# Optimization experiments

Hardware: AMD Instinct MI355X
Metric: run time of the kernel (lower is better)

The kernel has to match this reference:

```python
import jax, jax.numpy as jnp
import numpy as np

B, V, M, C = 1024, 2, 256, 256  # batch, num_vars (must be 2), latent states, categories


def setup_inputs() -> dict:
    key = jax.random.key(0)
    k1, k2, k3 = jax.random.split(key, 3)
    x = jax.random.randint(k1, (B, V), 0, C)
    # input-node tables: per var v, per latent node k, a [M, C] row-normalized table
    W = jax.nn.softmax(jax.random.normal(k2, (V, M, M, C), dtype=jnp.float32), axis=-1)
    # sum-node mixture weights over the M product children
    w_sum = jax.nn.softmax(jax.random.normal(k3, (M,), dtype=jnp.float32))
    return {"x": x, "W": W, "w_sum": w_sum}


def reference(x, W, w_sum):
    # lp[v] has shape [M(k), M(m), B]: log W[v, k, m, x[b, v]]
    # (matches torch: probs[:, x_var].log() per input node, stacked over latent k)
    lp0 = jnp.log(W[0][:, :, x[:, 0]])  # [M, M, B]
    lp1 = jnp.log(W[1][:, :, x[:, 1]])  # [M, M, B]
    prod = lp0 + lp1                    # product nodes, [M(k), M, B]
    # sum node: log( sum_k w_k * exp(prod_k) ) -> [M, B]
    mixed = jnp.log(jnp.einsum('k,kmb->mb', w_sum, jnp.exp(prod)))
    # root: logsumexp over the leading M dim -> [B]
    return jax.nn.logsumexp(mixed, axis=0)
```

## Files before the change

kernel.cpp:

```cpp
#include <hip/hip_runtime.h>
#include <math.h>


#define NBLK    256
#define KCHUNK  256
#define BK      64
#define NITER   (KCHUNK / BK)

typedef float  f32x4  __attribute__((ext_vector_type(4)));
typedef short  bf16x8 __attribute__((ext_vector_type(8)));

static __device__ __forceinline__ short f2bf(float f) {
    unsigned u = __builtin_bit_cast(unsigned, f);
    u += 0x7fffu + ((u >> 16) & 1u);
    return (short)(u >> 16);
}

static __device__ __forceinline__ int swz(int c) {
    return ((c >> 2) & 7) ^ ((c & 1) << 2);
}

__global__ __launch_bounds__(512, 2) void hclt_gemm(
    const int* __restrict__ x, const float* __restrict__ W,
    const float* __restrict__ wsum, float* __restrict__ P)
{
    __shared__ __align__(16) char smem[65536];
    __shared__ int pairs[1024];

    char*  const AsB = smem;
    char*  const BsB = smem + 32768;
    float* const G   = (float*)smem;

    const int  blk   = blockIdx.x;
    const long kbase = (long)blk * KCHUNK;
    const float wk   = wsum[blk];

    const float* __restrict__ Ag = W + kbase * 256;
    const float* __restrict__ Bg = W + 16777216 + kbase * 256;

    const int t    = threadIdx.x;
    const int lane = t & 63;
    const int wv   = t >> 6;

    {
        const int2 p0 = ((const int2*)x)[t];
        const int2 p1 = ((const int2*)x)[t + 512];
        pairs[t]       = (p0.x << 8) | p0.y;
        pairs[t + 512] = (p1.x << 8) | p1.y;
    }

    const int cq = lane * 4;
    const int g0 = wv;

    const int wc0 = (wv & 3) * 64;
    const int wc1 = (wv >> 2) * 128;
    const int ml  = lane & 15;
    const int qd  = lane >> 4;

    f32x4 acc[4][8];
#pragma unroll
    for (int i = 0; i < 4; ++i)
#pragma unroll
        for (int j = 0; j < 8; ++j) acc[i][j] = (f32x4){0.f, 0.f, 0.f, 0.f};

    float4 a4[8], b4[8];

#pragma unroll
    for (int r = 0; r < 8; ++r) {
        a4[r] = *(const float4*)(Ag + (long)(g0 * 8 + r) * 256 + cq);
        b4[r] = *(const float4*)(Bg + (long)(g0 * 8 + r) * 256 + cq);
    }
#pragma unroll
    for (int j = 0; j < 4; ++j) {
        const int c = cq + j;
        bf16x8 av, bv;
#pragma unroll
        for (int r = 0; r < 8; ++r) {
            av[r] = f2bf(((const float*)&a4[r])[j] * wk);
            bv[r] = f2bf(((const float*)&b4[r])[j]);
        }
        const int off = c * 128 + (g0 ^ swz(c)) * 16;
        *(bf16x8*)(AsB + off) = av;
        *(bf16x8*)(BsB + off) = bv;
    }
    __syncthreads();

#pragma unroll
    for (int it = 0; it < NITER; ++it) {
        if (it + 1 < NITER) {
#pragma unroll
            for (int r = 0; r < 8; ++r) {
                a4[r] = *(const float4*)(Ag + (long)((it + 1) * BK + g0 * 8 + r) * 256 + cq);
                b4[r] = *(const float4*)(Bg + (long)((it + 1) * BK + g0 * 8 + r) * 256 + cq);
            }
        }
#pragma unroll
        for (int s = 0; s < 2; ++s) {
            bf16x8 afr[4];
#pragma unroll
            for (int mi = 0; mi < 4; ++mi) {
                const int c = wc0 + mi * 16 + ml;
                afr[mi] = *(const bf16x8*)(AsB + c * 128 + (((s << 2) + qd) ^ swz(c)) * 16);
            }
#pragma unroll
            for (int ni = 0; ni < 8; ++ni) {
                const int c = wc1 + ni * 16 + ml;
                const bf16x8 bfr =
                    *(const bf16x8*)(BsB + c * 128 + (((s << 2) + qd) ^ swz(c)) * 16);
#pragma unroll
                for (int mi = 0; mi < 4; ++mi)
                    acc[mi][ni] = __builtin_amdgcn_mfma_f32_16x16x32_bf16(
                        afr[mi], bfr, acc[mi][ni], 0, 0, 0);
            }
        }
        if (it + 1 < NITER) {
            __syncthreads();
#pragma unroll
            for (int j = 0; j < 4; ++j) {
                const int c = cq + j;
                bf16x8 av, bv;
#pragma unroll
                for (int r = 0; r < 8; ++r) {
                    av[r] = f2bf(((const float*)&a4[r])[j] * wk);
                    bv[r] = f2bf(((const float*)&b4[r])[j]);
                }
                const int off = c * 128 + (g0 ^ swz(c)) * 16;
                *(bf16x8*)(AsB + off) = av;
                *(bf16x8*)(BsB + off) = bv;
            }
            __syncthreads();
        }
    }

    float v0 = 0.f, v1 = 0.f;
#pragma unroll 1
    for (int ph = 0; ph < 8; ++ph) {
        __syncthreads();
        if (wv == ph) {
#pragma unroll
            for (int mi = 0; mi < 4; ++mi)
#pragma unroll
                for (int ni = 0; ni < 8; ++ni)
#pragma unroll
                    for (int r = 0; r < 4; ++r)
                        G[(mi * 16 + qd * 4 + r) * 130 + (ni * 16 + ml)] = acc[mi][ni][r];
        }
        __syncthreads();
        {
            int pr = pairs[t];
            int c0 = pr >> 8, c1 = pr & 255;
            if ((((c0 >> 6) & 3) | ((c1 >> 7) << 2)) == ph)
                v0 = G[(c0 & 63) * 130 + (c1 & 127)];
            pr = pairs[t + 512];
            c0 = pr >> 8; c1 = pr & 255;
            if ((((c0 >> 6) & 3) | ((c1 >> 7) << 2)) == ph)
                v1 = G[(c0 & 63) * 130 + (c1 & 127)];
        }
    }
    P[(size_t)blk * 1024 + t]       = v0;
    P[(size_t)blk * 1024 + 512 + t] = v1;
}

__global__ __launch_bounds__(256) void hclt_finish(
    const float* __restrict__ P, float* __restrict__ out)
{
    const int i = blockIdx.x * 256 + threadIdx.x;
    float s0 = 0.f, s1 = 0.f, s2 = 0.f, s3 = 0.f;
#pragma unroll 8
    for (int s = 0; s < NBLK; s += 4) {
        s0 += P[(size_t)(s + 0) * 1024 + i];
        s1 += P[(size_t)(s + 1) * 1024 + i];
        s2 += P[(size_t)(s + 2) * 1024 + i];
        s3 += P[(size_t)(s + 3) * 1024 + i];
    }
    out[i] = logf((s0 + s1) + (s2 + s3));
}

extern "C" void kernel_launch(void* const* d_in, const int* in_sizes, int n_in,
                              void* d_out, int out_size, void* d_ws, size_t ws_size,
                              hipStream_t stream)
{
    const int*   x    = (const int*)d_in[0];
    const float* W    = (const float*)d_in[1];
    const float* wsum = (const float*)d_in[2];
    float* out = (float*)d_out;

    float* P = (float*)d_ws;

    hclt_gemm<<<dim3(NBLK), 512, 0, stream>>>(x, W, wsum, P);
    hclt_finish<<<dim3(4), 256, 0, stream>>>(P, out);
}
```

Baseline: 220.3 us.

## Split each k-chunk GEMM across two blocks by A-row halves, shrink tiles

Each k-chunk is now handled by two 256-thread blocks, each computing half of the A dimension (128 rows), giving 512 blocks instead of 256. The K tile shrinks to 32 with a new swizzle, and shared memory drops to about 33 KB. The wsum scaling moves from every bf16 conversion to the final gathered values, and the finish kernel is reworked to reduce over 512 partials with a shared-memory reduction across 16 blocks. This aims to raise occupancy and CU coverage on a 256-CU part, at the cost of B-tile loads duplicated across the two blocks of a pair and more synchronisation steps.

Result: slower. 227.5 us (+3.3%).

```diff
diff --git a/kernel.cpp b/kernel.cpp
--- a/kernel.cpp
+++ b/kernel.cpp
@@ -2,9 +2,8 @@
 #include <math.h>
 
 
-#define NBLK    256
 #define KCHUNK  256
-#define BK      64
+#define BK      32
 #define NITER   (KCHUNK / BK)
 
 typedef float  f32x4  __attribute__((ext_vector_type(4)));
@@ -16,44 +15,49 @@
     return (short)(u >> 16);
 }
 
-static __device__ __forceinline__ int swz(int c) {
-    return ((c >> 2) & 7) ^ ((c & 1) << 2);
-}
-
-__global__ __launch_bounds__(512, 2) void hclt_gemm(
+static __device__ __forceinline__ int s2(int c) {
+    return ((c >> 2) ^ ((c & 1) << 1)) & 3;
+}
+
+__global__ __launch_bounds__(256, 2) void hclt_gemm(
     const int* __restrict__ x, const float* __restrict__ W,
     const float* __restrict__ wsum, float* __restrict__ P)
 {
-    __shared__ __align__(16) char smem[65536];
+    __shared__ __align__(16) char smem[33280];
     __shared__ int pairs[1024];
 
-    char*  const AsB = smem;
-    char*  const BsB = smem + 32768;
-    float* const G   = (float*)smem;
-
-    const int  blk   = blockIdx.x;
-    const long kbase = (long)blk * KCHUNK;
-    const float wk   = wsum[blk];
-
-    const float* __restrict__ Ag = W + kbase * 256;
+    char*  const As = smem;
+    char*  const Bs = smem + 8192;
+    float* const G  = (float*)smem;
+
+    const int blk   = blockIdx.x;
+    const int split = ((blk >> 4) << 3) | (blk & 7);
+    const int h     = (blk >> 3) & 1;
+    const long kbase = (long)split * KCHUNK;
+
+    const float* __restrict__ Ag = W + kbase * 256 + h * 128;
     const float* __restrict__ Bg = W + 16777216 + kbase * 256;
 
     const int t    = threadIdx.x;
     const int lane = t & 63;
     const int wv   = t >> 6;
 
-    {
-        const int2 p0 = ((const int2*)x)[t];
-        const int2 p1 = ((const int2*)x)[t + 512];
-        pairs[t]       = (p0.x << 8) | p0.y;
-        pairs[t + 512] = (p1.x << 8) | p1.y;
-    }
-
-    const int cq = lane * 4;
-    const int g0 = wv;
-
-    const int wc0 = (wv & 3) * 64;
-    const int wc1 = (wv >> 2) * 128;
+#pragma unroll
+    for (int jj = 0; jj < 4; ++jj) {
+        const int2 p = ((const int2*)x)[t + 256 * jj];
+        pairs[t + 256 * jj] = (p.x << 8) | p.y;
+    }
+
+    const bool isA = (t < 128);
+    const int  uA  = t;
+    const int  cqA = (uA & 31) * 4;
+    const int  oA  = uA >> 5;
+    const int  vB  = t & 127;
+    const int  cqB = (vB & 63) * 4;
+    const int  oB  = (vB >> 6) * 2;
+
+    const int wc0 = (wv & 1) * 64;
+    const int wc1 = (wv >> 1) * 128;
     const int ml  = lane & 15;
     const int qd  = lane >> 4;
 
@@ -63,78 +67,106 @@
 #pragma unroll
         for (int j = 0; j < 8; ++j) acc[i][j] = (f32x4){0.f, 0.f, 0.f, 0.f};
 
-    float4 a4[8], b4[8];
-
-#pragma unroll
-    for (int r = 0; r < 8; ++r) {
-        a4[r] = *(const float4*)(Ag + (long)(g0 * 8 + r) * 256 + cq);
-        b4[r] = *(const float4*)(Bg + (long)(g0 * 8 + r) * 256 + cq);
-    }
-#pragma unroll
-    for (int j = 0; j < 4; ++j) {
-        const int c = cq + j;
-        bf16x8 av, bv;
-#pragma unroll
-        for (int r = 0; r < 8; ++r) {
-            av[r] = f2bf(((const float*)&a4[r])[j] * wk);
-            bv[r] = f2bf(((const float*)&b4[r])[j]);
-        }
-        const int off = c * 128 + (g0 ^ swz(c)) * 16;
-        *(bf16x8*)(AsB + off) = av;
-        *(bf16x8*)(BsB + off) = bv;
+    float4 pf[16];
+
+    if (isA) {
+#pragma unroll
+        for (int r = 0; r < 8; ++r)
+            pf[r] = *(const float4*)(Ag + (long)(oA * 8 + r) * 256 + cqA);
+    } else {
+#pragma unroll
+        for (int uo = 0; uo < 2; ++uo)
+#pragma unroll
+            for (int r = 0; r < 8; ++r)
+                pf[uo * 8 + r] = *(const float4*)(Bg + (long)((oB + uo) * 8 + r) * 256 + cqB);
+    }
+    if (isA) {
+#pragma unroll
+        for (int j = 0; j < 4; ++j) {
+            const int c = cqA + j;
+            bf16x8 av;
+#pragma unroll
+            for (int r = 0; r < 8; ++r) av[r] = f2bf(((const float*)&pf[r])[j]);
+            *(bf16x8*)(As + c * 64 + ((oA ^ s2(c)) & 3) * 16) = av;
+        }
+    } else {
+#pragma unroll
+        for (int uo = 0; uo < 2; ++uo)
+#pragma unroll
+            for (int j = 0; j < 4; ++j) {
+                const int c = cqB + j;
+                bf16x8 bv;
+#pragma unroll
+                for (int r = 0; r < 8; ++r) bv[r] = f2bf(((const float*)&pf[uo * 8 + r])[j]);
+                *(bf16x8*)(Bs + c * 64 + (((oB + uo) ^ s2(c)) & 3) * 16) = bv;
+            }
     }
     __syncthreads();
 
 #pragma unroll
     for (int it = 0; it < NITER; ++it) {
         if (it + 1 < NITER) {
-#pragma unroll
-            for (int r = 0; r < 8; ++r) {
-                a4[r] = *(const float4*)(Ag + (long)((it + 1) * BK + g0 * 8 + r) * 256 + cq);
-                b4[r] = *(const float4*)(Bg + (long)((it + 1) * BK + g0 * 8 + r) * 256 + cq);
-            }
-        }
-#pragma unroll
-        for (int s = 0; s < 2; ++s) {
-            bf16x8 afr[4];
-#pragma unroll
-            for (int mi = 0; mi < 4; ++mi) {
-                const int c = wc0 + mi * 16 + ml;
-                afr[mi] = *(const bf16x8*)(AsB + c * 128 + (((s << 2) + qd) ^ swz(c)) * 16);
-            }
-#pragma unroll
-            for (int ni = 0; ni < 8; ++ni) {
-                const int c = wc1 + ni * 16 + ml;
-                const bf16x8 bfr =
-                    *(const bf16x8*)(BsB + c * 128 + (((s << 2) + qd) ^ swz(c)) * 16);
-#pragma unroll
-                for (int mi = 0; mi < 4; ++mi)
-                    acc[mi][ni] = __builtin_amdgcn_mfma_f32_16x16x32_bf16(
-                        afr[mi], bfr, acc[mi][ni], 0, 0, 0);
-            }
+            const long k0 = (long)(it + 1) * BK;
+            if (isA) {
+#pragma unroll
+                for (int r = 0; r < 8; ++r)
+                    pf[r] = *(const float4*)(Ag + (k0 + oA * 8 + r) * 256 + cqA);
+            } else {
+#pragma unroll
+                for (int uo = 0; uo < 2; ++uo)
+#pragma unroll
+                    for (int r = 0; r < 8; ++r)
+                        pf[uo * 8 + r] =
+                            *(const float4*)(Bg + (k0 + (oB + uo) * 8 + r) * 256 + cqB);
+            }
+        }
+        bf16x8 afr[4];
+#pragma unroll
+        for (int mi = 0; mi < 4; ++mi) {
+            const int c = wc0 + mi * 16 + ml;
+            afr[mi] = *(const bf16x8*)(As + c * 64 + ((qd ^ s2(c)) & 3) * 16);
+        }
+#pragma unroll
+        for (int ni = 0; ni < 8; ++ni) {
+            const int c = wc1 + ni * 16 + ml;
+            const bf16x8 bfr = *(const bf16x8*)(Bs + c * 64 + ((qd ^ s2(c)) & 3) * 16);
+#pragma unroll
+            for (int mi = 0; mi < 4; ++mi)
+                acc[mi][ni] = __builtin_amdgcn_mfma_f32_16x16x32_bf16(
+                    afr[mi], bfr, acc[mi][ni], 0, 0, 0);
         }
         if (it + 1 < NITER) {
             __syncthreads();
-#pragma unroll
-            for (int j = 0; j < 4; ++j) {
-                const int c = cq + j;
-                bf16x8 av, bv;
-#pragma unroll
-                for (int r = 0; r < 8; ++r) {
-                    av[r] = f2bf(((const float*)&a4[r])[j] * wk);
-                    bv[r] = f2bf(((const float*)&b4[r])[j]);
+            if (isA) {
+#pragma unroll
+                for (int j = 0; j < 4; ++j) {
+                    const int c = cqA + j;
+                    bf16x8 av;
+#pragma unroll
+                    for (int r = 0; r < 8; ++r) av[r] = f2bf(((const float*)&pf[r])[j]);
+                    *(bf16x8*)(As + c * 64 + ((oA ^ s2(c)) & 3) * 16) = av;
                 }
-                const int off = c * 128 + (g0 ^ swz(c)) * 16;
-                *(bf16x8*)(AsB + off) = av;
-                *(bf16x8*)(BsB + off) = bv;
+            } else {
+#pragma unroll
+                for (int uo = 0; uo < 2; ++uo)
+#pragma unroll
+                    for (int j = 0; j < 4; ++j) {
+                        const int c = cqB + j;
+                        bf16x8 bv;
+#pragma unroll
+                        for (int r = 0; r < 8; ++r)
+                            bv[r] = f2bf(((const float*)&pf[uo * 8 + r])[j]);
+                        *(bf16x8*)(Bs + c * 64 + (((oB + uo) ^ s2(c)) & 3) * 16) = bv;
+                    }
             }
             __syncthreads();
         }
     }
 
-    float v0 = 0.f, v1 = 0.f;
+    const float wk = wsum[split];
+    float pv0 = 0.f, pv1 = 0.f, pv2 = 0.f, pv3 = 0.f;
 #pragma unroll 1
-    for (int ph = 0; ph < 8; ++ph) {
+    for (int ph = 0; ph < 4; ++ph) {
         __syncthreads();
         if (wv == ph) {
 #pragma unroll
@@ -146,34 +178,39 @@
                         G[(mi * 16 + qd * 4 + r) * 130 + (ni * 16 + ml)] = acc[mi][ni][r];
         }
         __syncthreads();
-        {
-            int pr = pairs[t];
-            int c0 = pr >> 8, c1 = pr & 255;
-            if ((((c0 >> 6) & 3) | ((c1 >> 7) << 2)) == ph)
-                v0 = G[(c0 & 63) * 130 + (c1 & 127)];
-            pr = pairs[t + 512];
-            c0 = pr >> 8; c1 = pr & 255;
-            if ((((c0 >> 6) & 3) | ((c1 >> 7) << 2)) == ph)
-                v1 = G[(c0 & 63) * 130 + (c1 & 127)];
-        }
-    }
-    P[(size_t)blk * 1024 + t]       = v0;
-    P[(size_t)blk * 1024 + 512 + t] = v1;
+#pragma unroll
+        for (int jj = 0; jj < 4; ++jj) {
+            const int pr = pairs[t + 256 * jj];
+            const int c0 = pr >> 8, c1 = pr & 255;
+            if ((c0 >> 7) == h && ((((c0 >> 6) & 1) | ((c1 >> 7) << 1)) == ph)) {
+                const float v = G[(c0 & 63) * 130 + (c1 & 127)];
+                if (jj == 0) pv0 = v; else if (jj == 1) pv1 = v;
+                else if (jj == 2) pv2 = v; else pv3 = v;
+            }
+        }
+    }
+    float* __restrict__ Pb = P + (size_t)blk * 1024;
+    Pb[t]       = pv0 * wk;
+    Pb[t + 256] = pv1 * wk;
+    Pb[t + 512] = pv2 * wk;
+    Pb[t + 768] = pv3 * wk;
 }
 
 __global__ __launch_bounds__(256) void hclt_finish(
     const float* __restrict__ P, float* __restrict__ out)
 {
-    const int i = blockIdx.x * 256 + threadIdx.x;
-    float s0 = 0.f, s1 = 0.f, s2 = 0.f, s3 = 0.f;
+    __shared__ float red[4][64];
+    const int l = threadIdx.x & 63;
+    const int q = threadIdx.x >> 6;
+    const int i = blockIdx.x * 64 + l;
+    float s = 0.f;
 #pragma unroll 8
-    for (int s = 0; s < NBLK; s += 4) {
-        s0 += P[(size_t)(s + 0) * 1024 + i];
-        s1 += P[(size_t)(s + 1) * 1024 + i];
-        s2 += P[(size_t)(s + 2) * 1024 + i];
-        s3 += P[(size_t)(s + 3) * 1024 + i];
-    }
-    out[i] = logf((s0 + s1) + (s2 + s3));
+    for (int m = 0; m < 128; ++m)
+        s += P[(size_t)(q + 4 * m) * 1024 + i];
+    red[q][l] = s;
+    __syncthreads();
+    if (q == 0)
+        out[i] = logf((red[0][l] + red[1][l]) + (red[2][l] + red[3][l]));
 }
 
 extern "C" void kernel_launch(void* const* d_in, const int* in_sizes, int n_in,
@@ -187,6 +224,6 @@
 
     float* P = (float*)d_ws;
 
-    hclt_gemm<<<dim3(NBLK), 512, 0, stream>>>(x, W, wsum, P);
-    hclt_finish<<<dim3(4), 256, 0, stream>>>(P, out);
-}
+    hclt_gemm<<<dim3(512), 256, 0, stream>>>(x, W, wsum, P);
+    hclt_finish<<<dim3(16), 256, 0, stream>>>(P, out);
+}
```
